# Kernel optimization log

Hardware: AMD Instinct MI355X
Metric: run time of the kernel (lower is better)

## Reference

```python
import jax, jax.numpy as jnp
import numpy as np

WIN = 7          # window height/width
NUM_HEADS = 12
DIM = 384
B_WINDOWS = 4096  # num_windows * batch


def make_relative_position_index(wh, ww):
    # Exact replica of the Swin precomputed index buffer.
    coords = np.stack(np.meshgrid(np.arange(wh), np.arange(ww), indexing='ij'))  # (2,wh,ww)
    coords = coords.reshape(2, -1)                                               # (2, wh*ww)
    rel = coords[:, :, None] - coords[:, None, :]                                # (2, N, N)
    rel = rel.transpose(1, 2, 0).astype(np.int64)                                # (N, N, 2)
    rel[:, :, 0] += wh - 1
    rel[:, :, 1] += ww - 1
    rel[:, :, 0] *= 2 * ww - 1
    return rel.sum(-1).astype(np.int32)                                          # (N, N)


def setup_inputs() -> dict:
    key = jax.random.key(0)
    ks = jax.random.split(key, 6)
    N = WIN * WIN
    table_rows = (2 * WIN - 1) * (2 * WIN - 1)  # 169
    inv = 1.0 / np.sqrt(DIM)
    x = jax.random.normal(ks[0], (B_WINDOWS, N, DIM), dtype=jnp.float32)
    qkv_w = jax.random.normal(ks[1], (3 * DIM, DIM), dtype=jnp.float32) * inv
    qkv_b = jnp.zeros((3 * DIM,), dtype=jnp.float32)
    proj_w = jax.random.normal(ks[2], (DIM, DIM), dtype=jnp.float32) * inv
    proj_b = jnp.zeros((DIM,), dtype=jnp.float32)
    bias_table = jax.random.normal(ks[3], (table_rows, NUM_HEADS), dtype=jnp.float32) * 0.02
    rel_index = jnp.asarray(make_relative_position_index(WIN, WIN))
    return {"x": x, "qkv_w": qkv_w, "qkv_b": qkv_b, "proj_w": proj_w,
            "proj_b": proj_b, "bias_table": bias_table, "rel_index": rel_index}


def reference(x, qkv_w, qkv_b, proj_w, proj_b, bias_table, rel_index):
    B_, N, C = x.shape
    H = NUM_HEADS
    hd = C // H
    scale = hd ** (-0.5)
    # qkv projection: (B_, N, 3C) -> (3, B_, H, N, hd)
    qkv = (jnp.einsum('bnc,oc->bno', x, qkv_w) + qkv_b)
    qkv = qkv.reshape(B_, N, 3, H, hd).transpose(2, 0, 3, 1, 4)
    q, k, v = qkv[0], qkv[1], qkv[2]
    attn = jnp.einsum('bhnd,bhmd->bhnm', q * scale, k)          # (B_, H, N, N)
    # gathered relative position bias: (N, N, H) -> (H, N, N)
    bias = bias_table[rel_index.reshape(-1)].reshape(N, N, H).transpose(2, 0, 1)
    attn = jax.nn.softmax(attn + bias[None], axis=-1)
    out = jnp.einsum('bhnm,bhmd->bnhd', attn, v).reshape(B_, N, C)
    out = jnp.einsum('bnc,oc->bno', out, proj_w) + proj_b
    return out
```

## Files before the change

kernel.cpp:

```cpp
#include <hip/hip_runtime.h>

typedef __bf16 bf16x8 __attribute__((ext_vector_type(8)));
typedef float f32x4 __attribute__((ext_vector_type(4)));
typedef unsigned short u16;
typedef unsigned int u32;

#define WIN_N 49
#define CDIM 384
#define NHEADS 12
#define HDIM 32
#define SCALE 0.17677669529663687f

__device__ __forceinline__ u16 f2bf(float f) {
  u32 u = __float_as_uint(f);
  u32 r = (u + 0x7FFFu + ((u >> 16) & 1u)) >> 16;
  return (u16)r;
}

__device__ __forceinline__ bf16x8 ld_frag(const u16* base, int row, int nrows,
                                          int stride, int k0, int quad) {
  bf16x8 z = {};
  if (row < nrows)
    z = *(const bf16x8*)(base + row * stride + k0 + quad * 8);
  return z;
}

__global__ void prep_kernel(const float* __restrict__ qkv_w,
                            const float* __restrict__ proj_w,
                            const float* __restrict__ bias_table,
                            const int* __restrict__ rel_index,
                            u16* __restrict__ qkvWb, u16* __restrict__ projWb,
                            float* __restrict__ biasF) {
  int i = blockIdx.x * blockDim.x + threadIdx.x;
  int stride = gridDim.x * blockDim.x;
  for (int t = i; t < 3 * CDIM * CDIM; t += stride) qkvWb[t] = f2bf(qkv_w[t]);
  for (int t = i; t < CDIM * CDIM; t += stride) projWb[t] = f2bf(proj_w[t]);
  for (int t = i; t < NHEADS * WIN_N * WIN_N; t += stride) {
    int h = t / (WIN_N * WIN_N);
    int r = t - h * (WIN_N * WIN_N);
    biasF[t] = bias_table[rel_index[r] * NHEADS + h];
  }
}

__global__ void __launch_bounds__(256, 2)
swin_fused(const float* __restrict__ x, const float* __restrict__ qkv_b,
           const float* __restrict__ proj_b, const u16* __restrict__ qkvWb,
           const u16* __restrict__ projWb, const float* __restrict__ biasF,
           float* __restrict__ out) {
  __shared__ __align__(16) u16 sm[34400];
  u16* Xb = sm;
  u16* Qb = sm + 19208;
  u16* Kb = sm + 22736;
  u16* Pb = sm + 19208;
  u16* Vt = sm + 26264;
  u16* Og = sm + 30872;

  const int tid = threadIdx.x;
  const int w = tid >> 6, lane = tid & 63, quad = lane >> 4, l16 = lane & 15;
  const int b = blockIdx.x;
  const int mhalf = w & 1, hh = w >> 1;

  const float4* xs = (const float4*)(x + (size_t)b * (WIN_N * CDIM));
  for (int i = tid; i < WIN_N * (CDIM / 4); i += 256) {
    int m = i / 96, c4 = (i - m * 96) * 4;
    float4 v = xs[i];
    u32* dst = (u32*)(Xb + m * 392 + c4);
    dst[0] = (u32)f2bf(v.x) | ((u32)f2bf(v.y) << 16);
    dst[1] = (u32)f2bf(v.z) | ((u32)f2bf(v.w) << 16);
  }
  for (int i = tid; i < (64 * 72) / 2; i += 256) ((u32*)Vt)[i] = 0u;

  f32x4 pacc[6][4];
#pragma unroll
  for (int t = 0; t < 6; ++t)
#pragma unroll
    for (int mt = 0; mt < 4; ++mt) pacc[t][mt] = (f32x4){0.f, 0.f, 0.f, 0.f};

  for (int g = 0; g < 6; ++g) {
    __syncthreads();

    int mat[3], hhc[3], half[3], orow[3];
#pragma unroll
    for (int tl = 0; tl < 3; ++tl) {
      int t = w * 3 + tl;
      int chunk = t >> 1;
      half[tl] = t & 1;
      mat[tl] = chunk >> 1;
      hhc[tl] = chunk & 1;
      orow[tl] = mat[tl] * CDIM + (g * 2 + hhc[tl]) * HDIM + half[tl] * 16 + l16;
    }
    f32x4 acc[3][4];
#pragma unroll
    for (int tl = 0; tl < 3; ++tl)
#pragma unroll
      for (int mt = 0; mt < 4; ++mt) acc[tl][mt] = (f32x4){0.f, 0.f, 0.f, 0.f};

    for (int k = 0; k < 12; ++k) {
      bf16x8 a[4];
#pragma unroll
      for (int mt = 0; mt < 4; ++mt)
        a[mt] = ld_frag(Xb, mt * 16 + l16, WIN_N, 392, k * 32, quad);
#pragma unroll
      for (int tl = 0; tl < 3; ++tl) {
        bf16x8 bw = *(const bf16x8*)(qkvWb + (size_t)orow[tl] * CDIM + k * 32 + quad * 8);
#pragma unroll
        for (int mt = 0; mt < 4; ++mt)
          acc[tl][mt] = __builtin_amdgcn_mfma_f32_16x16x32_bf16(a[mt], bw, acc[tl][mt], 0, 0, 0);
      }
    }
#pragma unroll
    for (int tl = 0; tl < 3; ++tl) {
      float bias = qkv_b[orow[tl]];
      int col = hhc[tl] * HDIM + half[tl] * 16 + l16;
#pragma unroll
      for (int mt = 0; mt < 4; ++mt)
#pragma unroll
        for (int r = 0; r < 4; ++r) {
          int tok = mt * 16 + quad * 4 + r;
          if (tok < WIN_N) {
            u16 hv = f2bf(acc[tl][mt][r] + bias);
            if (mat[tl] == 0)      Qb[tok * 72 + col] = hv;
            else if (mat[tl] == 1) Kb[tok * 72 + col] = hv;
            else                   Vt[col * 72 + tok] = hv;
          }
        }
    }
    __syncthreads();

    f32x4 S[2][4];
    bf16x8 aq[2];
#pragma unroll
    for (int mt2 = 0; mt2 < 2; ++mt2)
      aq[mt2] = ld_frag(Qb, (2 * mhalf + mt2) * 16 + l16, WIN_N, 72, hh * HDIM, quad);
#pragma unroll
    for (int nt = 0; nt < 4; ++nt) {
      bf16x8 bk = ld_frag(Kb, nt * 16 + l16, WIN_N, 72, hh * HDIM, quad);
#pragma unroll
      for (int mt2 = 0; mt2 < 2; ++mt2) {
        f32x4 z = (f32x4){0.f, 0.f, 0.f, 0.f};
        S[mt2][nt] = __builtin_amdgcn_mfma_f32_16x16x32_bf16(aq[mt2], bk, z, 0, 0, 0);
      }
    }
    const int hglob = g * 2 + hh;
#pragma unroll
    for (int mt2 = 0; mt2 < 2; ++mt2)
#pragma unroll
      for (int r = 0; r < 4; ++r) {
        int m = (2 * mhalf + mt2) * 16 + quad * 4 + r;
        float v[4];
#pragma unroll
        for (int nt = 0; nt < 4; ++nt) {
          int n = nt * 16 + l16;
          float s;
          if (m < WIN_N && n < WIN_N)
            s = S[mt2][nt][r] * SCALE + biasF[(hglob * WIN_N + m) * WIN_N + n];
          else
            s = (m >= WIN_N) ? 0.f : -1e30f;
          v[nt] = s;
        }
        float mx = fmaxf(fmaxf(v[0], v[1]), fmaxf(v[2], v[3]));
        mx = fmaxf(mx, __shfl_xor(mx, 1));
        mx = fmaxf(mx, __shfl_xor(mx, 2));
        mx = fmaxf(mx, __shfl_xor(mx, 4));
        mx = fmaxf(mx, __shfl_xor(mx, 8));
        float sum = 0.f;
#pragma unroll
        for (int nt = 0; nt < 4; ++nt) {
          v[nt] = __expf(v[nt] - mx);
          sum += v[nt];
        }
        sum += __shfl_xor(sum, 1);
        sum += __shfl_xor(sum, 2);
        sum += __shfl_xor(sum, 4);
        sum += __shfl_xor(sum, 8);
        float inv = 1.f / sum;
#pragma unroll
        for (int nt = 0; nt < 4; ++nt) S[mt2][nt][r] = v[nt] * inv;
      }
    __syncthreads();

    u16* Ph = Pb + hh * 3528;
#pragma unroll
    for (int mt2 = 0; mt2 < 2; ++mt2)
#pragma unroll
      for (int nt = 0; nt < 4; ++nt)
#pragma unroll
        for (int r = 0; r < 4; ++r) {
          int m = (2 * mhalf + mt2) * 16 + quad * 4 + r;
          if (m < WIN_N) Ph[m * 72 + nt * 16 + l16] = f2bf(S[mt2][nt][r]);
        }
    __syncthreads();

    f32x4 o2[2][2];
#pragma unroll
    for (int mt2 = 0; mt2 < 2; ++mt2)
#pragma unroll
      for (int nt2 = 0; nt2 < 2; ++nt2) o2[mt2][nt2] = (f32x4){0.f, 0.f, 0.f, 0.f};
    bf16x8 bv[2][2];
#pragma unroll
    for (int nt2 = 0; nt2 < 2; ++nt2)
#pragma unroll
      for (int kk = 0; kk < 2; ++kk)
        bv[nt2][kk] = ld_frag(Vt, hh * HDIM + nt2 * 16 + l16, 64, 72, kk * 32, quad);
#pragma unroll
    for (int mt2 = 0; mt2 < 2; ++mt2)
#pragma unroll
      for (int kk = 0; kk < 2; ++kk) {
        bf16x8 ap = ld_frag(Ph, (2 * mhalf + mt2) * 16 + l16, WIN_N, 72, kk * 32, quad);
#pragma unroll
        for (int nt2 = 0; nt2 < 2; ++nt2)
          o2[mt2][nt2] = __builtin_amdgcn_mfma_f32_16x16x32_bf16(ap, bv[nt2][kk], o2[mt2][nt2], 0, 0, 0);
      }
#pragma unroll
    for (int mt2 = 0; mt2 < 2; ++mt2)
#pragma unroll
      for (int nt2 = 0; nt2 < 2; ++nt2)
#pragma unroll
        for (int r = 0; r < 4; ++r) {
          int tok = (2 * mhalf + mt2) * 16 + quad * 4 + r;
          if (tok < WIN_N)
            Og[tok * 72 + hh * HDIM + nt2 * 16 + l16] = f2bf(o2[mt2][nt2][r]);
        }
    __syncthreads();

#pragma unroll
    for (int kk = 0; kk < 2; ++kk) {
      bf16x8 ao[4];
#pragma unroll
      for (int mt = 0; mt < 4; ++mt)
        ao[mt] = ld_frag(Og, mt * 16 + l16, WIN_N, 72, kk * 32, quad);
#pragma unroll
      for (int t6 = 0; t6 < 6; ++t6) {
        int nrow = w * 96 + t6 * 16 + l16;
        bf16x8 bw = *(const bf16x8*)(projWb + (size_t)nrow * CDIM + g * 64 + kk * 32 + quad * 8);
#pragma unroll
        for (int mt = 0; mt < 4; ++mt)
          pacc[t6][mt] = __builtin_amdgcn_mfma_f32_16x16x32_bf16(ao[mt], bw, pacc[t6][mt], 0, 0, 0);
      }
    }
  }

  float* outp = out + (size_t)b * (WIN_N * CDIM);
#pragma unroll
  for (int t6 = 0; t6 < 6; ++t6) {
    int n = w * 96 + t6 * 16 + l16;
    float pb = proj_b[n];
#pragma unroll
    for (int mt = 0; mt < 4; ++mt)
#pragma unroll
      for (int r = 0; r < 4; ++r) {
        int m = mt * 16 + quad * 4 + r;
        if (m < WIN_N) outp[m * CDIM + n] = pacc[t6][mt][r] + pb;
      }
  }
}

extern "C" void kernel_launch(void* const* d_in, const int* in_sizes, int n_in,
                              void* d_out, int out_size, void* d_ws, size_t ws_size,
                              hipStream_t stream) {
  const float* x          = (const float*)d_in[0];
  const float* qkv_w      = (const float*)d_in[1];
  const float* qkv_b      = (const float*)d_in[2];
  const float* proj_w     = (const float*)d_in[3];
  const float* proj_b     = (const float*)d_in[4];
  const float* bias_table = (const float*)d_in[5];
  const int*   rel_index  = (const int*)d_in[6];

  u16* qkvWb = (u16*)d_ws;
  u16* projWb = qkvWb + 3 * CDIM * CDIM;
  float* biasF = (float*)(projWb + CDIM * CDIM);

  hipLaunchKernelGGL(prep_kernel, dim3(512), dim3(256), 0, stream,
                     qkv_w, proj_w, bias_table, rel_index, qkvWb, projWb, biasF);
  hipLaunchKernelGGL(swin_fused, dim3(4096), dim3(256), 0, stream,
                     x, qkv_b, proj_b, qkvWb, projWb, biasF, (float*)d_out);
}
```

Before: 1.718 ms.

## Split fused Swin kernel into bf16 staging, attention, and projection kernels

The single fused kernel is split into three. A prep pass converts x to bf16 into scratch space inside the output buffer. An attention kernel reads X from global memory and writes per-head outputs back to global. A separate projection kernel then computes the output projection in place. Shared memory per block drops, launch bounds rise, and two barriers inside the attention loop are removed, all aimed at higher occupancy and shorter sync chains. The cost is extra global round-trips for X and the attention output, repeated global reads of X in every head-group iteration, and two more kernel launches.

```diff
diff --git a/kernel.cpp b/kernel.cpp
--- a/kernel.cpp
+++ b/kernel.cpp
@@ -10,6 +10,7 @@
 #define NHEADS 12
 #define HDIM 32
 #define SCALE 0.17677669529663687f
+#define WTOK (WIN_N * CDIM)
 
 __device__ __forceinline__ u16 f2bf(float f) {
   u32 u = __float_as_uint(f);
@@ -21,16 +22,17 @@
                                           int stride, int k0, int quad) {
   bf16x8 z = {};
   if (row < nrows)
-    z = *(const bf16x8*)(base + row * stride + k0 + quad * 8);
+    z = *(const bf16x8*)(base + (size_t)row * stride + k0 + quad * 8);
   return z;
 }
 
-__global__ void prep_kernel(const float* __restrict__ qkv_w,
+__global__ void prep_kernel(const float* __restrict__ x,
+                            const float* __restrict__ qkv_w,
                             const float* __restrict__ proj_w,
                             const float* __restrict__ bias_table,
                             const int* __restrict__ rel_index,
                             u16* __restrict__ qkvWb, u16* __restrict__ projWb,
-                            float* __restrict__ biasF) {
+                            float* __restrict__ biasF, float* __restrict__ out) {
   int i = blockIdx.x * blockDim.x + threadIdx.x;
   int stride = gridDim.x * blockDim.x;
   for (int t = i; t < 3 * CDIM * CDIM; t += stride) qkvWb[t] = f2bf(qkv_w[t]);
@@ -40,55 +42,54 @@
     int r = t - h * (WIN_N * WIN_N);
     biasF[t] = bias_table[rel_index[r] * NHEADS + h];
   }
-}
-
-__global__ void __launch_bounds__(256, 2)
-swin_fused(const float* __restrict__ x, const float* __restrict__ qkv_b,
-           const float* __restrict__ proj_b, const u16* __restrict__ qkvWb,
-           const u16* __restrict__ projWb, const float* __restrict__ biasF,
-           float* __restrict__ out) {
-  __shared__ __align__(16) u16 sm[34400];
-  u16* Xb = sm;
-  u16* Qb = sm + 19208;
-  u16* Kb = sm + 22736;
-  u16* Pb = sm + 19208;
-  u16* Vt = sm + 26264;
-  u16* Og = sm + 30872;
+  const float4* xv = (const float4*)x;
+  for (u32 t = (u32)i; t < 4096u * 4704u; t += (u32)stride) {
+    u32 b = t / 4704u, r = t - b * 4704u;
+    float4 v = xv[t];
+    u32* dst = (u32*)((u16*)(out + (size_t)b * WTOK) + r * 4u);
+    dst[0] = (u32)f2bf(v.x) | ((u32)f2bf(v.y) << 16);
+    dst[1] = (u32)f2bf(v.z) | ((u32)f2bf(v.w) << 16);
+  }
+}
+
+__global__ void __launch_bounds__(256, 4)
+swin_attn(const float* __restrict__ qkv_b, const u16* __restrict__ qkvWb,
+          const float* __restrict__ biasF, float* __restrict__ out) {
+  __shared__ __align__(16) u16 sm[18720];
+  u16* Qb = sm;
+  u16* Kb = sm + 3528;
+  u16* Vt = sm + 7056;
+  u16* Pb = sm + 11664;
 
   const int tid = threadIdx.x;
   const int w = tid >> 6, lane = tid & 63, quad = lane >> 4, l16 = lane & 15;
   const int b = blockIdx.x;
   const int mhalf = w & 1, hh = w >> 1;
 
-  const float4* xs = (const float4*)(x + (size_t)b * (WIN_N * CDIM));
-  for (int i = tid; i < WIN_N * (CDIM / 4); i += 256) {
-    int m = i / 96, c4 = (i - m * 96) * 4;
-    float4 v = xs[i];
-    u32* dst = (u32*)(Xb + m * 392 + c4);
-    dst[0] = (u32)f2bf(v.x) | ((u32)f2bf(v.y) << 16);
-    dst[1] = (u32)f2bf(v.z) | ((u32)f2bf(v.w) << 16);
-  }
+  u16* winBase = (u16*)(out + (size_t)b * WTOK);
+  const u16* Xg = winBase;
+  u16* Ao = winBase + WTOK;
+
   for (int i = tid; i < (64 * 72) / 2; i += 256) ((u32*)Vt)[i] = 0u;
 
-  f32x4 pacc[6][4];
-#pragma unroll
-  for (int t = 0; t < 6; ++t)
-#pragma unroll
-    for (int mt = 0; mt < 4; ++mt) pacc[t][mt] = (f32x4){0.f, 0.f, 0.f, 0.f};
+  int mat[3], hhc[3], half[3];
+#pragma unroll
+  for (int tl = 0; tl < 3; ++tl) {
+    int t = w * 3 + tl;
+    int chunk = t >> 1;
+    half[tl] = t & 1;
+    mat[tl] = chunk >> 1;
+    hhc[tl] = chunk & 1;
+  }
 
   for (int g = 0; g < 6; ++g) {
     __syncthreads();
 
-    int mat[3], hhc[3], half[3], orow[3];
-#pragma unroll
-    for (int tl = 0; tl < 3; ++tl) {
-      int t = w * 3 + tl;
-      int chunk = t >> 1;
-      half[tl] = t & 1;
-      mat[tl] = chunk >> 1;
-      hhc[tl] = chunk & 1;
+    int orow[3];
+#pragma unroll
+    for (int tl = 0; tl < 3; ++tl)
       orow[tl] = mat[tl] * CDIM + (g * 2 + hhc[tl]) * HDIM + half[tl] * 16 + l16;
-    }
+
     f32x4 acc[3][4];
 #pragma unroll
     for (int tl = 0; tl < 3; ++tl)
@@ -99,7 +100,7 @@
       bf16x8 a[4];
 #pragma unroll
       for (int mt = 0; mt < 4; ++mt)
-        a[mt] = ld_frag(Xb, mt * 16 + l16, WIN_N, 392, k * 32, quad);
+        a[mt] = ld_frag(Xg, mt * 16 + l16, WIN_N, CDIM, k * 32, quad);
 #pragma unroll
       for (int tl = 0; tl < 3; ++tl) {
         bf16x8 bw = *(const bf16x8*)(qkvWb + (size_t)orow[tl] * CDIM + k * 32 + quad * 8);
@@ -177,7 +178,6 @@
 #pragma unroll
         for (int nt = 0; nt < 4; ++nt) S[mt2][nt][r] = v[nt] * inv;
       }
-    __syncthreads();
 
     u16* Ph = Pb + hh * 3528;
 #pragma unroll
@@ -189,7 +189,6 @@
           int m = (2 * mhalf + mt2) * 16 + quad * 4 + r;
           if (m < WIN_N) Ph[m * 72 + nt * 16 + l16] = f2bf(S[mt2][nt][r]);
         }
-    __syncthreads();
 
     f32x4 o2[2][2];
 #pragma unroll
@@ -219,38 +218,52 @@
         for (int r = 0; r < 4; ++r) {
           int tok = (2 * mhalf + mt2) * 16 + quad * 4 + r;
           if (tok < WIN_N)
-            Og[tok * 72 + hh * HDIM + nt2 * 16 + l16] = f2bf(o2[mt2][nt2][r]);
-        }
-    __syncthreads();
-
-#pragma unroll
-    for (int kk = 0; kk < 2; ++kk) {
-      bf16x8 ao[4];
+            Ao[tok * CDIM + hglob * HDIM + nt2 * 16 + l16] = f2bf(o2[mt2][nt2][r]);
+        }
+  }
+}
+
+__global__ void __launch_bounds__(512, 4)
+swin_proj(const float* __restrict__ proj_b, const u16* __restrict__ projWb,
+          float* __restrict__ out) {
+  const int tid = threadIdx.x;
+  const int w = tid >> 6, lane = tid & 63, quad = lane >> 4, l16 = lane & 15;
+  const int b = blockIdx.x;
+  const u16* Ain = (const u16*)(out + (size_t)b * WTOK) + WTOK;
+
+  f32x4 pacc[3][4];
+#pragma unroll
+  for (int t3 = 0; t3 < 3; ++t3)
+#pragma unroll
+    for (int mt = 0; mt < 4; ++mt) pacc[t3][mt] = (f32x4){0.f, 0.f, 0.f, 0.f};
+
+  for (int k = 0; k < 12; ++k) {
+    bf16x8 a[4];
+#pragma unroll
+    for (int mt = 0; mt < 4; ++mt)
+      a[mt] = ld_frag(Ain, mt * 16 + l16, WIN_N, CDIM, k * 32, quad);
+#pragma unroll
+    for (int t3 = 0; t3 < 3; ++t3) {
+      int nrow = w * 48 + t3 * 16 + l16;
+      bf16x8 bw = *(const bf16x8*)(projWb + (size_t)nrow * CDIM + k * 32 + quad * 8);
 #pragma unroll
       for (int mt = 0; mt < 4; ++mt)
-        ao[mt] = ld_frag(Og, mt * 16 + l16, WIN_N, 72, kk * 32, quad);
-#pragma unroll
-      for (int t6 = 0; t6 < 6; ++t6) {
-        int nrow = w * 96 + t6 * 16 + l16;
-        bf16x8 bw = *(const bf16x8*)(projWb + (size_t)nrow * CDIM + g * 64 + kk * 32 + quad * 8);
-#pragma unroll
-        for (int mt = 0; mt < 4; ++mt)
-          pacc[t6][mt] = __builtin_amdgcn_mfma_f32_16x16x32_bf16(ao[mt], bw, pacc[t6][mt], 0, 0, 0);
-      }
-    }
-  }
-
-  float* outp = out + (size_t)b * (WIN_N * CDIM);
-#pragma unroll
-  for (int t6 = 0; t6 < 6; ++t6) {
-    int n = w * 96 + t6 * 16 + l16;
+        pacc[t3][mt] = __builtin_amdgcn_mfma_f32_16x16x32_bf16(a[mt], bw, pacc[t3][mt], 0, 0, 0);
+    }
+  }
+  __syncthreads();
+
+  float* outp = out + (size_t)b * WTOK;
+#pragma unroll
+  for (int t3 = 0; t3 < 3; ++t3) {
+    int n = w * 48 + t3 * 16 + l16;
     float pb = proj_b[n];
 #pragma unroll
     for (int mt = 0; mt < 4; ++mt)
 #pragma unroll
       for (int r = 0; r < 4; ++r) {
         int m = mt * 16 + quad * 4 + r;
-        if (m < WIN_N) outp[m * CDIM + n] = pacc[t6][mt][r] + pb;
+        if (m < WIN_N) outp[m * CDIM + n] = pacc[t3][mt][r] + pb;
       }
   }
 }
@@ -270,8 +283,11 @@
   u16* projWb = qkvWb + 3 * CDIM * CDIM;
   float* biasF = (float*)(projWb + CDIM * CDIM);
 
-  hipLaunchKernelGGL(prep_kernel, dim3(512), dim3(256), 0, stream,
-                     qkv_w, proj_w, bias_table, rel_index, qkvWb, projWb, biasF);
-  hipLaunchKernelGGL(swin_fused, dim3(4096), dim3(256), 0, stream,
-                     x, qkv_b, proj_b, qkvWb, projWb, biasF, (float*)d_out);
-}
+  hipLaunchKernelGGL(prep_kernel, dim3(2048), dim3(256), 0, stream,
+                     x, qkv_w, proj_w, bias_table, rel_index, qkvWb, projWb, biasF,
+                     (float*)d_out);
+  hipLaunchKernelGGL(swin_attn, dim3(4096), dim3(256), 0, stream,
+                     qkv_b, qkvWb, biasF, (float*)d_out);
+  hipLaunchKernelGGL(swin_proj, dim3(4096), dim3(512), 0, stream,
+                     proj_b, projWb, (float*)d_out);
+}
```

After: 2.229 ms. +29.7%, slower.

## Split fused Swin window kernel across eight waves instead of four

Applied to the files above, without the earlier changes.

Raises the block from 256 to 512 threads and divides each stage's work over eight wavefronts. QKV tiles are now split by token tile and output half, attention by head and row tile, and projection columns by 48 per wave. The relative-position bias is loaded before the QK MFMAs, and one barrier between the P write and the PV product is dropped, which is safe because each wave only reads its own P rows. This halves per-thread accumulator registers so more waves can hide latency, at the cost of more redundant weight fragment loads from global memory per block.

```diff
diff --git a/kernel.cpp b/kernel.cpp
--- a/kernel.cpp
+++ b/kernel.cpp
@@ -10,6 +10,7 @@
 #define NHEADS 12
 #define HDIM 32
 #define SCALE 0.17677669529663687f
+#define WTOK (WIN_N * CDIM)
 
 __device__ __forceinline__ u16 f2bf(float f) {
   u32 u = __float_as_uint(f);
@@ -42,7 +43,7 @@
   }
 }
 
-__global__ void __launch_bounds__(256, 2)
+__global__ void __launch_bounds__(512, 4)
 swin_fused(const float* __restrict__ x, const float* __restrict__ qkv_b,
            const float* __restrict__ proj_b, const u16* __restrict__ qkvWb,
            const u16* __restrict__ projWb, const float* __restrict__ biasF,
@@ -58,199 +59,182 @@
   const int tid = threadIdx.x;
   const int w = tid >> 6, lane = tid & 63, quad = lane >> 4, l16 = lane & 15;
   const int b = blockIdx.x;
-  const int mhalf = w & 1, hh = w >> 1;
-
-  const float4* xs = (const float4*)(x + (size_t)b * (WIN_N * CDIM));
-  for (int i = tid; i < WIN_N * (CDIM / 4); i += 256) {
+  const int mt = w >> 1, nh = w & 1;
+  const int hh = w >> 2, amt = w & 3;
+
+  const float4* xs = (const float4*)(x + (size_t)b * WTOK);
+  for (int i = tid; i < WIN_N * 96; i += 512) {
     int m = i / 96, c4 = (i - m * 96) * 4;
     float4 v = xs[i];
     u32* dst = (u32*)(Xb + m * 392 + c4);
     dst[0] = (u32)f2bf(v.x) | ((u32)f2bf(v.y) << 16);
     dst[1] = (u32)f2bf(v.z) | ((u32)f2bf(v.w) << 16);
   }
-  for (int i = tid; i < (64 * 72) / 2; i += 256) ((u32*)Vt)[i] = 0u;
-
-  f32x4 pacc[6][4];
-#pragma unroll
-  for (int t = 0; t < 6; ++t)
-#pragma unroll
-    for (int mt = 0; mt < 4; ++mt) pacc[t][mt] = (f32x4){0.f, 0.f, 0.f, 0.f};
+  for (int i = tid; i < (64 * 72) / 2; i += 512) ((u32*)Vt)[i] = 0u;
+
+  int matv[6], colv[6], rowb[6];
+#pragma unroll
+  for (int j = 0; j < 6; ++j) {
+    int t = nh * 6 + j;
+    int chunk = t >> 1, half = t & 1;
+    matv[j] = chunk >> 1;
+    int hhc = chunk & 1;
+    colv[j] = hhc * HDIM + half * 16 + l16;
+    rowb[j] = matv[j] * CDIM + hhc * HDIM + half * 16 + l16;
+  }
+
+  f32x4 pacc[3][4];
+#pragma unroll
+  for (int t3 = 0; t3 < 3; ++t3)
+#pragma unroll
+    for (int m4 = 0; m4 < 4; ++m4) pacc[t3][m4] = (f32x4){0.f, 0.f, 0.f, 0.f};
 
   for (int g = 0; g < 6; ++g) {
     __syncthreads();
 
-    int mat[3], hhc[3], half[3], orow[3];
-#pragma unroll
-    for (int tl = 0; tl < 3; ++tl) {
-      int t = w * 3 + tl;
-      int chunk = t >> 1;
-      half[tl] = t & 1;
-      mat[tl] = chunk >> 1;
-      hhc[tl] = chunk & 1;
-      orow[tl] = mat[tl] * CDIM + (g * 2 + hhc[tl]) * HDIM + half[tl] * 16 + l16;
-    }
-    f32x4 acc[3][4];
-#pragma unroll
-    for (int tl = 0; tl < 3; ++tl)
-#pragma unroll
-      for (int mt = 0; mt < 4; ++mt) acc[tl][mt] = (f32x4){0.f, 0.f, 0.f, 0.f};
+    f32x4 acc[6];
+#pragma unroll
+    for (int j = 0; j < 6; ++j) acc[j] = (f32x4){0.f, 0.f, 0.f, 0.f};
 
     for (int k = 0; k < 12; ++k) {
-      bf16x8 a[4];
-#pragma unroll
-      for (int mt = 0; mt < 4; ++mt)
-        a[mt] = ld_frag(Xb, mt * 16 + l16, WIN_N, 392, k * 32, quad);
-#pragma unroll
-      for (int tl = 0; tl < 3; ++tl) {
-        bf16x8 bw = *(const bf16x8*)(qkvWb + (size_t)orow[tl] * CDIM + k * 32 + quad * 8);
-#pragma unroll
-        for (int mt = 0; mt < 4; ++mt)
-          acc[tl][mt] = __builtin_amdgcn_mfma_f32_16x16x32_bf16(a[mt], bw, acc[tl][mt], 0, 0, 0);
-      }
-    }
-#pragma unroll
-    for (int tl = 0; tl < 3; ++tl) {
-      float bias = qkv_b[orow[tl]];
-      int col = hhc[tl] * HDIM + half[tl] * 16 + l16;
-#pragma unroll
-      for (int mt = 0; mt < 4; ++mt)
-#pragma unroll
-        for (int r = 0; r < 4; ++r) {
-          int tok = mt * 16 + quad * 4 + r;
-          if (tok < WIN_N) {
-            u16 hv = f2bf(acc[tl][mt][r] + bias);
-            if (mat[tl] == 0)      Qb[tok * 72 + col] = hv;
-            else if (mat[tl] == 1) Kb[tok * 72 + col] = hv;
-            else                   Vt[col * 72 + tok] = hv;
-          }
+      bf16x8 a = ld_frag(Xb, mt * 16 + l16, WIN_N, 392, k * 32, quad);
+#pragma unroll
+      for (int j = 0; j < 6; ++j) {
+        bf16x8 bw = *(const bf16x8*)(qkvWb + (size_t)(rowb[j] + g * 64) * CDIM + k * 32 + quad * 8);
+        acc[j] = __builtin_amdgcn_mfma_f32_16x16x32_bf16(a, bw, acc[j], 0, 0, 0);
+      }
+    }
+#pragma unroll
+    for (int j = 0; j < 6; ++j) {
+      float bias = qkv_b[rowb[j] + g * 64];
+      int col = colv[j];
+#pragma unroll
+      for (int r = 0; r < 4; ++r) {
+        int tok = mt * 16 + quad * 4 + r;
+        if (tok < WIN_N) {
+          u16 hv = f2bf(acc[j][r] + bias);
+          if (matv[j] == 0)      Qb[tok * 72 + col] = hv;
+          else if (matv[j] == 1) Kb[tok * 72 + col] = hv;
+          else                   Vt[col * 72 + tok] = hv;
         }
-    }
-    __syncthreads();
-
-    f32x4 S[2][4];
-    bf16x8 aq[2];
-#pragma unroll
-    for (int mt2 = 0; mt2 < 2; ++mt2)
-      aq[mt2] = ld_frag(Qb, (2 * mhalf + mt2) * 16 + l16, WIN_N, 72, hh * HDIM, quad);
+      }
+    }
+    __syncthreads();
+
+    bf16x8 aq = ld_frag(Qb, amt * 16 + l16, WIN_N, 72, hh * HDIM, quad);
+    bf16x8 bk[4];
+#pragma unroll
+    for (int nt = 0; nt < 4; ++nt)
+      bk[nt] = ld_frag(Kb, nt * 16 + l16, WIN_N, 72, hh * HDIM, quad);
+
+    const int hglob = g * 2 + hh;
+    const float* bp = biasF + (size_t)hglob * WIN_N * WIN_N;
+    float bl[4][4];
+#pragma unroll
+    for (int r = 0; r < 4; ++r) {
+      int m = amt * 16 + quad * 4 + r;
+#pragma unroll
+      for (int nt = 0; nt < 4; ++nt) {
+        int n = nt * 16 + l16;
+        bl[r][nt] = (m < WIN_N && n < WIN_N) ? bp[m * WIN_N + n]
+                                             : ((m >= WIN_N) ? 0.f : -1e30f);
+      }
+    }
+
+    f32x4 S[4];
 #pragma unroll
     for (int nt = 0; nt < 4; ++nt) {
-      bf16x8 bk = ld_frag(Kb, nt * 16 + l16, WIN_N, 72, hh * HDIM, quad);
-#pragma unroll
-      for (int mt2 = 0; mt2 < 2; ++mt2) {
-        f32x4 z = (f32x4){0.f, 0.f, 0.f, 0.f};
-        S[mt2][nt] = __builtin_amdgcn_mfma_f32_16x16x32_bf16(aq[mt2], bk, z, 0, 0, 0);
-      }
-    }
-    const int hglob = g * 2 + hh;
-#pragma unroll
-    for (int mt2 = 0; mt2 < 2; ++mt2)
-#pragma unroll
-      for (int r = 0; r < 4; ++r) {
-        int m = (2 * mhalf + mt2) * 16 + quad * 4 + r;
-        float v[4];
-#pragma unroll
-        for (int nt = 0; nt < 4; ++nt) {
-          int n = nt * 16 + l16;
-          float s;
-          if (m < WIN_N && n < WIN_N)
-            s = S[mt2][nt][r] * SCALE + biasF[(hglob * WIN_N + m) * WIN_N + n];
-          else
-            s = (m >= WIN_N) ? 0.f : -1e30f;
-          v[nt] = s;
-        }
-        float mx = fmaxf(fmaxf(v[0], v[1]), fmaxf(v[2], v[3]));
-        mx = fmaxf(mx, __shfl_xor(mx, 1));
-        mx = fmaxf(mx, __shfl_xor(mx, 2));
-        mx = fmaxf(mx, __shfl_xor(mx, 4));
-        mx = fmaxf(mx, __shfl_xor(mx, 8));
-        float sum = 0.f;
-#pragma unroll
-        for (int nt = 0; nt < 4; ++nt) {
-          v[nt] = __expf(v[nt] - mx);
-          sum += v[nt];
-        }
-        sum += __shfl_xor(sum, 1);
-        sum += __shfl_xor(sum, 2);
-        sum += __shfl_xor(sum, 4);
-        sum += __shfl_xor(sum, 8);
-        float inv = 1.f / sum;
-#pragma unroll
-        for (int nt = 0; nt < 4; ++nt) S[mt2][nt][r] = v[nt] * inv;
-      }
+      f32x4 z = (f32x4){0.f, 0.f, 0.f, 0.f};
+      S[nt] = __builtin_amdgcn_mfma_f32_16x16x32_bf16(aq, bk[nt], z, 0, 0, 0);
+    }
+
+#pragma unroll
+    for (int r = 0; r < 4; ++r) {
+      float v[4];
+#pragma unroll
+      for (int nt = 0; nt < 4; ++nt) v[nt] = S[nt][r] * SCALE + bl[r][nt];
+      float mx = fmaxf(fmaxf(v[0], v[1]), fmaxf(v[2], v[3]));
+      mx = fmaxf(mx, __shfl_xor(mx, 1));
+      mx = fmaxf(mx, __shfl_xor(mx, 2));
+      mx = fmaxf(mx, __shfl_xor(mx, 4));
+      mx = fmaxf(mx, __shfl_xor(mx, 8));
+      float sum = 0.f;
+#pragma unroll
+      for (int nt = 0; nt < 4; ++nt) {
+        v[nt] = __expf(v[nt] - mx);
+        sum += v[nt];
+      }
+      sum += __shfl_xor(sum, 1);
+      sum += __shfl_xor(sum, 2);
+      sum += __shfl_xor(sum, 4);
+      sum += __shfl_xor(sum, 8);
+      float inv = 1.f / sum;
+#pragma unroll
+      for (int nt = 0; nt < 4; ++nt) S[nt][r] = v[nt] * inv;
+    }
     __syncthreads();
 
     u16* Ph = Pb + hh * 3528;
 #pragma unroll
-    for (int mt2 = 0; mt2 < 2; ++mt2)
-#pragma unroll
-      for (int nt = 0; nt < 4; ++nt)
-#pragma unroll
-        for (int r = 0; r < 4; ++r) {
-          int m = (2 * mhalf + mt2) * 16 + quad * 4 + r;
-          if (m < WIN_N) Ph[m * 72 + nt * 16 + l16] = f2bf(S[mt2][nt][r]);
-        }
-    __syncthreads();
-
-    f32x4 o2[2][2];
-#pragma unroll
-    for (int mt2 = 0; mt2 < 2; ++mt2)
-#pragma unroll
-      for (int nt2 = 0; nt2 < 2; ++nt2) o2[mt2][nt2] = (f32x4){0.f, 0.f, 0.f, 0.f};
-    bf16x8 bv[2][2];
+    for (int nt = 0; nt < 4; ++nt)
+#pragma unroll
+      for (int r = 0; r < 4; ++r) {
+        int m = amt * 16 + quad * 4 + r;
+        if (m < WIN_N) Ph[m * 72 + nt * 16 + l16] = f2bf(S[nt][r]);
+      }
+
+    f32x4 o2[2];
+    o2[0] = (f32x4){0.f, 0.f, 0.f, 0.f};
+    o2[1] = (f32x4){0.f, 0.f, 0.f, 0.f};
+    bf16x8 ap[2];
+#pragma unroll
+    for (int kk = 0; kk < 2; ++kk)
+      ap[kk] = ld_frag(Ph, amt * 16 + l16, WIN_N, 72, kk * 32, quad);
+#pragma unroll
+    for (int kk = 0; kk < 2; ++kk)
+#pragma unroll
+      for (int nt2 = 0; nt2 < 2; ++nt2) {
+        bf16x8 bv = ld_frag(Vt, hh * HDIM + nt2 * 16 + l16, 64, 72, kk * 32, quad);
+        o2[nt2] = __builtin_amdgcn_mfma_f32_16x16x32_bf16(ap[kk], bv, o2[nt2], 0, 0, 0);
+      }
 #pragma unroll
     for (int nt2 = 0; nt2 < 2; ++nt2)
 #pragma unroll
-      for (int kk = 0; kk < 2; ++kk)
-        bv[nt2][kk] = ld_frag(Vt, hh * HDIM + nt2 * 16 + l16, 64, 72, kk * 32, quad);
-#pragma unroll
-    for (int mt2 = 0; mt2 < 2; ++mt2)
-#pragma unroll
-      for (int kk = 0; kk < 2; ++kk) {
-        bf16x8 ap = ld_frag(Ph, (2 * mhalf + mt2) * 16 + l16, WIN_N, 72, kk * 32, quad);
-#pragma unroll
-        for (int nt2 = 0; nt2 < 2; ++nt2)
-          o2[mt2][nt2] = __builtin_amdgcn_mfma_f32_16x16x32_bf16(ap, bv[nt2][kk], o2[mt2][nt2], 0, 0, 0);
-      }
-#pragma unroll
-    for (int mt2 = 0; mt2 < 2; ++mt2)
-#pragma unroll
-      for (int nt2 = 0; nt2 < 2; ++nt2)
-#pragma unroll
-        for (int r = 0; r < 4; ++r) {
-          int tok = (2 * mhalf + mt2) * 16 + quad * 4 + r;
-          if (tok < WIN_N)
-            Og[tok * 72 + hh * HDIM + nt2 * 16 + l16] = f2bf(o2[mt2][nt2][r]);
-        }
+      for (int r = 0; r < 4; ++r) {
+        int tok = amt * 16 + quad * 4 + r;
+        if (tok < WIN_N)
+          Og[tok * 72 + hh * HDIM + nt2 * 16 + l16] = f2bf(o2[nt2][r]);
+      }
     __syncthreads();
 
 #pragma unroll
     for (int kk = 0; kk < 2; ++kk) {
       bf16x8 ao[4];
 #pragma unroll
-      for (int mt = 0; mt < 4; ++mt)
-        ao[mt] = ld_frag(Og, mt * 16 + l16, WIN_N, 72, kk * 32, quad);
-#pragma unroll
-      for (int t6 = 0; t6 < 6; ++t6) {
-        int nrow = w * 96 + t6 * 16 + l16;
+      for (int m4 = 0; m4 < 4; ++m4)
+        ao[m4] = ld_frag(Og, m4 * 16 + l16, WIN_N, 72, kk * 32, quad);
+#pragma unroll
+      for (int t3 = 0; t3 < 3; ++t3) {
+        int nrow = w * 48 + t3 * 16 + l16;
         bf16x8 bw = *(const bf16x8*)(projWb + (size_t)nrow * CDIM + g * 64 + kk * 32 + quad * 8);
 #pragma unroll
-        for (int mt = 0; mt < 4; ++mt)
-          pacc[t6][mt] = __builtin_amdgcn_mfma_f32_16x16x32_bf16(ao[mt], bw, pacc[t6][mt], 0, 0, 0);
-      }
-    }
-  }
-
-  float* outp = out + (size_t)b * (WIN_N * CDIM);
-#pragma unroll
-  for (int t6 = 0; t6 < 6; ++t6) {
-    int n = w * 96 + t6 * 16 + l16;
+        for (int m4 = 0; m4 < 4; ++m4)
+          pacc[t3][m4] = __builtin_amdgcn_mfma_f32_16x16x32_bf16(ao[m4], bw, pacc[t3][m4], 0, 0, 0);
+      }
+    }
+  }
+
+  float* outp = out + (size_t)b * WTOK;
+#pragma unroll
+  for (int t3 = 0; t3 < 3; ++t3) {
+    int n = w * 48 + t3 * 16 + l16;
     float pb = proj_b[n];
 #pragma unroll
-    for (int mt = 0; mt < 4; ++mt)
-#pragma unroll
-      for (int r = 0; r < 4; ++r) {
-        int m = mt * 16 + quad * 4 + r;
-        if (m < WIN_N) outp[m * CDIM + n] = pacc[t6][mt][r] + pb;
+    for (int m4 = 0; m4 < 4; ++m4)
+#pragma unroll
+      for (int r = 0; r < 4; ++r) {
+        int m = m4 * 16 + quad * 4 + r;
+        if (m < WIN_N) outp[m * CDIM + n] = pacc[t3][m4][r] + pb;
       }
   }
 }
@@ -272,6 +256,6 @@
 
   hipLaunchKernelGGL(prep_kernel, dim3(512), dim3(256), 0, stream,
                      qkv_w, proj_w, bias_table, rel_index, qkvWb, projWb, biasF);
-  hipLaunchKernelGGL(swin_fused, dim3(4096), dim3(256), 0, stream,
+  hipLaunchKernelGGL(swin_fused, dim3(4096), dim3(512), 0, stream,
                      x, qkv_b, proj_b, qkvWb, projWb, biasF, (float*)d_out);
 }
```

After: 2.912 ms. +69.5%, slower.

## Prefetch weights and bias into registers and drop a redundant barrier

Applied to the files above, without the earlier changes.

Global loads of QKV weights are double-buffered in registers across the k loop, which is now fully unrolled. The relative-position bias for each head group is preloaded before the QKV GEMM, and the projection weight fragments are loaded before the barrier so their latency overlaps other work. The barrier between writing P and the PV MMA is removed, since each wave reads only the P rows it wrote itself. Register pressure rises sharply (pacc, acc, bias cache and weight buffers), which may lower occupancy or cause spills.

```diff
diff --git a/kernel.cpp b/kernel.cpp
--- a/kernel.cpp
+++ b/kernel.cpp
@@ -70,47 +70,87 @@
   }
   for (int i = tid; i < (64 * 72) / 2; i += 256) ((u32*)Vt)[i] = 0u;
 
+  int mat[3], hhc[3], half[3], rowb[3];
+#pragma unroll
+  for (int tl = 0; tl < 3; ++tl) {
+    int t = w * 3 + tl;
+    int chunk = t >> 1;
+    half[tl] = t & 1;
+    mat[tl] = chunk >> 1;
+    hhc[tl] = chunk & 1;
+    rowb[tl] = mat[tl] * CDIM + hhc[tl] * HDIM + half[tl] * 16 + l16;
+  }
+
   f32x4 pacc[6][4];
 #pragma unroll
-  for (int t = 0; t < 6; ++t)
-#pragma unroll
-    for (int mt = 0; mt < 4; ++mt) pacc[t][mt] = (f32x4){0.f, 0.f, 0.f, 0.f};
+  for (int t6 = 0; t6 < 6; ++t6)
+#pragma unroll
+    for (int mt = 0; mt < 4; ++mt) pacc[t6][mt] = (f32x4){0.f, 0.f, 0.f, 0.f};
+
+#define LOADW(dst, kk)                                                        \
+  _Pragma("unroll") for (int tl = 0; tl < 3; ++tl) dst[tl] =                  \
+      *(const bf16x8*)(qkvWb + (size_t)(rowb[tl] + g * 64) * CDIM + (kk)*32 + \
+                       quad * 8);
 
   for (int g = 0; g < 6; ++g) {
+    const int hglob = g * 2 + hh;
+    const float* bp = biasF + (size_t)hglob * WIN_N * WIN_N;
+    float bl[2][4][4];
+#pragma unroll
+    for (int mt2 = 0; mt2 < 2; ++mt2)
+#pragma unroll
+      for (int r = 0; r < 4; ++r) {
+        int m = (2 * mhalf + mt2) * 16 + quad * 4 + r;
+#pragma unroll
+        for (int nt = 0; nt < 4; ++nt) {
+          int n = nt * 16 + l16;
+          bl[mt2][r][nt] = (m < WIN_N && n < WIN_N)
+                               ? bp[m * WIN_N + n]
+                               : ((m >= WIN_N) ? 0.f : -1e30f);
+        }
+      }
+    bf16x8 bwA[3], bwB[3];
+    LOADW(bwA, 0);
+
     __syncthreads();
 
-    int mat[3], hhc[3], half[3], orow[3];
+    f32x4 acc[3][4];
+#pragma unroll
+    for (int tl = 0; tl < 3; ++tl)
+#pragma unroll
+      for (int mt = 0; mt < 4; ++mt) acc[tl][mt] = (f32x4){0.f, 0.f, 0.f, 0.f};
+
+#pragma unroll
+    for (int k2 = 0; k2 < 6; ++k2) {
+      const int k0 = 2 * k2, k1 = 2 * k2 + 1;
+      LOADW(bwB, k1);
+      {
+        bf16x8 a[4];
+#pragma unroll
+        for (int mt = 0; mt < 4; ++mt)
+          a[mt] = ld_frag(Xb, mt * 16 + l16, WIN_N, 392, k0 * 32, quad);
+#pragma unroll
+        for (int tl = 0; tl < 3; ++tl)
+#pragma unroll
+          for (int mt = 0; mt < 4; ++mt)
+            acc[tl][mt] = __builtin_amdgcn_mfma_f32_16x16x32_bf16(a[mt], bwA[tl], acc[tl][mt], 0, 0, 0);
+      }
+      if (k2 < 5) LOADW(bwA, k0 + 2);
+      {
+        bf16x8 a[4];
+#pragma unroll
+        for (int mt = 0; mt < 4; ++mt)
+          a[mt] = ld_frag(Xb, mt * 16 + l16, WIN_N, 392, k1 * 32, quad);
+#pragma unroll
+        for (int tl = 0; tl < 3; ++tl)
+#pragma unroll
+          for (int mt = 0; mt < 4; ++mt)
+            acc[tl][mt] = __builtin_amdgcn_mfma_f32_16x16x32_bf16(a[mt], bwB[tl], acc[tl][mt], 0, 0, 0);
+      }
+    }
 #pragma unroll
     for (int tl = 0; tl < 3; ++tl) {
-      int t = w * 3 + tl;
-      int chunk = t >> 1;
-      half[tl] = t & 1;
-      mat[tl] = chunk >> 1;
-      hhc[tl] = chunk & 1;
-      orow[tl] = mat[tl] * CDIM + (g * 2 + hhc[tl]) * HDIM + half[tl] * 16 + l16;
-    }
-    f32x4 acc[3][4];
-#pragma unroll
-    for (int tl = 0; tl < 3; ++tl)
-#pragma unroll
-      for (int mt = 0; mt < 4; ++mt) acc[tl][mt] = (f32x4){0.f, 0.f, 0.f, 0.f};
-
-    for (int k = 0; k < 12; ++k) {
-      bf16x8 a[4];
-#pragma unroll
-      for (int mt = 0; mt < 4; ++mt)
-        a[mt] = ld_frag(Xb, mt * 16 + l16, WIN_N, 392, k * 32, quad);
-#pragma unroll
-      for (int tl = 0; tl < 3; ++tl) {
-        bf16x8 bw = *(const bf16x8*)(qkvWb + (size_t)orow[tl] * CDIM + k * 32 + quad * 8);
-#pragma unroll
-        for (int mt = 0; mt < 4; ++mt)
-          acc[tl][mt] = __builtin_amdgcn_mfma_f32_16x16x32_bf16(a[mt], bw, acc[tl][mt], 0, 0, 0);
-      }
-    }
-#pragma unroll
-    for (int tl = 0; tl < 3; ++tl) {
-      float bias = qkv_b[orow[tl]];
+      float bias = qkv_b[rowb[tl] + g * 64];
       int col = hhc[tl] * HDIM + half[tl] * 16 + l16;
 #pragma unroll
       for (int mt = 0; mt < 4; ++mt)
@@ -141,23 +181,13 @@
         S[mt2][nt] = __builtin_amdgcn_mfma_f32_16x16x32_bf16(aq[mt2], bk, z, 0, 0, 0);
       }
     }
-    const int hglob = g * 2 + hh;
 #pragma unroll
     for (int mt2 = 0; mt2 < 2; ++mt2)
 #pragma unroll
       for (int r = 0; r < 4; ++r) {
-        int m = (2 * mhalf + mt2) * 16 + quad * 4 + r;
         float v[4];
 #pragma unroll
-        for (int nt = 0; nt < 4; ++nt) {
-          int n = nt * 16 + l16;
-          float s;
-          if (m < WIN_N && n < WIN_N)
-            s = S[mt2][nt][r] * SCALE + biasF[(hglob * WIN_N + m) * WIN_N + n];
-          else
-            s = (m >= WIN_N) ? 0.f : -1e30f;
-          v[nt] = s;
-        }
+        for (int nt = 0; nt < 4; ++nt) v[nt] = S[mt2][nt][r] * SCALE + bl[mt2][r][nt];
         float mx = fmaxf(fmaxf(v[0], v[1]), fmaxf(v[2], v[3]));
         mx = fmaxf(mx, __shfl_xor(mx, 1));
         mx = fmaxf(mx, __shfl_xor(mx, 2));
@@ -189,7 +219,6 @@
           int m = (2 * mhalf + mt2) * 16 + quad * 4 + r;
           if (m < WIN_N) Ph[m * 72 + nt * 16 + l16] = f2bf(S[mt2][nt][r]);
         }
-    __syncthreads();
 
     f32x4 o2[2][2];
 #pragma unroll
@@ -221,22 +250,39 @@
           if (tok < WIN_N)
             Og[tok * 72 + hh * HDIM + nt2 * 16 + l16] = f2bf(o2[mt2][nt2][r]);
         }
+
+    bf16x8 pb0[6];
+#pragma unroll
+    for (int t6 = 0; t6 < 6; ++t6)
+      pb0[t6] = *(const bf16x8*)(projWb + (size_t)(w * 96 + t6 * 16 + l16) * CDIM + g * 64 + quad * 8);
+
     __syncthreads();
 
-#pragma unroll
-    for (int kk = 0; kk < 2; ++kk) {
+    bf16x8 pb1[6];
+#pragma unroll
+    for (int t6 = 0; t6 < 6; ++t6)
+      pb1[t6] = *(const bf16x8*)(projWb + (size_t)(w * 96 + t6 * 16 + l16) * CDIM + g * 64 + 32 + quad * 8);
+    {
       bf16x8 ao[4];
 #pragma unroll
       for (int mt = 0; mt < 4; ++mt)
-        ao[mt] = ld_frag(Og, mt * 16 + l16, WIN_N, 72, kk * 32, quad);
-#pragma unroll
-      for (int t6 = 0; t6 < 6; ++t6) {
-        int nrow = w * 96 + t6 * 16 + l16;
-        bf16x8 bw = *(const bf16x8*)(projWb + (size_t)nrow * CDIM + g * 64 + kk * 32 + quad * 8);
+        ao[mt] = ld_frag(Og, mt * 16 + l16, WIN_N, 72, 0, quad);
+#pragma unroll
+      for (int t6 = 0; t6 < 6; ++t6)
 #pragma unroll
         for (int mt = 0; mt < 4; ++mt)
-          pacc[t6][mt] = __builtin_amdgcn_mfma_f32_16x16x32_bf16(ao[mt], bw, pacc[t6][mt], 0, 0, 0);
-      }
+          pacc[t6][mt] = __builtin_amdgcn_mfma_f32_16x16x32_bf16(ao[mt], pb0[t6], pacc[t6][mt], 0, 0, 0);
+    }
+    {
+      bf16x8 ao[4];
+#pragma unroll
+      for (int mt = 0; mt < 4; ++mt)
+        ao[mt] = ld_frag(Og, mt * 16 + l16, WIN_N, 72, 32, quad);
+#pragma unroll
+      for (int t6 = 0; t6 < 6; ++t6)
+#pragma unroll
+        for (int mt = 0; mt < 4; ++mt)
+          pacc[t6][mt] = __builtin_amdgcn_mfma_f32_16x16x32_bf16(ao[mt], pb1[t6], pacc[t6][mt], 0, 0, 0);
     }
   }
 
```

Measured after the change: 2.089 ms. +21.6%, slower.
